# Kernel optimization log

Measured on AMD Instinct MI355X. Metric: run time of the kernel, lower is better.

Reference implementation:

```python
import jax, jax.numpy as jnp
import numpy as np

N_E = 1024
E_DIM = 64
BETA = 0.25
DECAY = 0.99
EPSILON = 1e-5


def setup_inputs() -> dict:
    key = jax.random.key(0)
    k1, k2, k3 = jax.random.split(key, 3)
    z = jax.random.normal(k1, (32, E_DIM, 32, 32), dtype=jnp.float32)
    # codebook initialized uniform(-1/n_e, 1/n_e) as in the torch module
    emb_w = jax.random.uniform(k2, (N_E, E_DIM), minval=-1.0 / N_E, maxval=1.0 / N_E, dtype=jnp.float32)
    ema_cluster_size = jnp.ones((N_E,), dtype=jnp.float32)
    ema_w = jax.random.uniform(k3, (N_E, E_DIM), minval=-1.0 / N_E, maxval=1.0 / N_E, dtype=jnp.float32)
    return {"z": z, "emb_w": emb_w, "ema_cluster_size": ema_cluster_size, "ema_w": ema_w}


def reference(z, emb_w, ema_cluster_size, ema_w):
    B, C, H, W = z.shape  # C == E_DIM
    zf = jnp.transpose(z, (0, 2, 3, 1)).reshape(-1, E_DIM)  # [N, e_dim]
    N = zf.shape[0]

    # squared-distance via ||z||^2 + ||e||^2 - 2 z.e (same expansion as torch code)
    d = (jnp.sum(zf * zf, axis=1, keepdims=True)
         + jnp.sum(emb_w * emb_w, axis=1)
         - 2.0 * zf @ emb_w.T)  # [N, n_e]
    idx = jnp.argmin(d, axis=1)  # [N]

    min_encodings = jax.nn.one_hot(idx, N_E, dtype=jnp.float32)  # [N, n_e]
    # cluster stats via scatter-add (equivalent to one-hot matmuls, cheaper)
    cluster_size = jax.ops.segment_sum(jnp.ones((N,), jnp.float32), idx, num_segments=N_E)
    sum_encodings = jax.ops.segment_sum(zf, idx, num_segments=N_E)  # [n_e, e_dim]

    # EMA update (training path, done before the z_q lookup as in torch)
    new_cs = DECAY * ema_cluster_size + (1.0 - DECAY) * cluster_size
    new_w = DECAY * ema_w + (1.0 - DECAY) * sum_encodings
    n = jnp.sum(new_cs)
    cs_norm = (new_cs + EPSILON) / (n + N_E * EPSILON) * n
    new_emb = new_w / cs_norm[:, None]  # updated codebook

    z_q = new_emb[idx].reshape(B, H, W, C).transpose(0, 3, 1, 2)  # [B,C,H,W]
    loss = BETA * jnp.mean((jax.lax.stop_gradient(z_q) - z) ** 2)
    z_q_st = z + jax.lax.stop_gradient(z_q - z)  # straight-through

    avg_probs = cluster_size / N
    perplexity = jnp.exp(-jnp.sum(avg_probs * jnp.log(avg_probs + 1e-10)))
    return loss, z_q_st, perplexity, min_encodings, idx
```

## Files before the change

### kernel.cpp

```cpp
#include <hip/hip_runtime.h>
#include <math.h>

#define NVEC 32768
#define NE   1024
#define ED   64
#define TOT  2097152
#define NCHUNK 4
#define CHUNK  256
#define MT     128

#define O_LOSS   0
#define O_ZQ     1
#define O_PERP   2097153
#define O_MINENC 2097154
#define O_IDX    35651586

#define W_PIDX   0
#define W_CS     32768
#define W_SUMENC 33792
#define W_NEWEMB 99328
#define W_ESQ    164864


__global__ void __launch_bounds__(256) k_pre(const float* __restrict__ emb,
                                             float* __restrict__ ws,
                                             float* __restrict__ out) {
    int b = blockIdx.x;
    if (b < 65) {
        int i = b * 256 + threadIdx.x;
        float4 zv; zv.x = 0.f; zv.y = 0.f; zv.z = 0.f; zv.w = 0.f;
        *(float4*)(ws + W_CS + i * 4) = zv;
        if (b == 0 && threadIdx.x == 0) out[O_LOSS] = 0.f;
    } else {
        int code = (b - 65) * 256 + threadIdx.x;
        const float* ep = emb + (size_t)code * ED;
        float r[8];
#pragma unroll
        for (int j = 0; j < 8; ++j) r[j] = __fmul_rn(ep[j], ep[j]);
#pragma unroll
        for (int i = 8; i < 64; i += 8)
#pragma unroll
            for (int j = 0; j < 8; ++j)
                r[j] = __fadd_rn(r[j], __fmul_rn(ep[i + j], ep[i + j]));
        ws[W_ESQ + code] = __fadd_rn(
            __fadd_rn(__fadd_rn(r[0], r[1]), __fadd_rn(r[2], r[3])),
            __fadd_rn(__fadd_rn(r[4], r[5]), __fadd_rn(r[6], r[7])));
    }
}

__device__ __forceinline__ int apos(int m) {
    return ((m & 4) << 4) + ((m >> 3) << 2) + (m & 3);
}

__global__ void __launch_bounds__(512) k_dist(const float* __restrict__ z,
                                              const float* __restrict__ emb,
                                              const float* __restrict__ esq_g,
                                              int* __restrict__ fidx,
                                              int* __restrict__ cnt,
                                              float* __restrict__ sumenc,
                                              float* __restrict__ out) {
    __shared__ __align__(16) float s_a[64 * 128];
    __shared__ __align__(16) float s_b[2 * 64 * 132];
    __shared__ float s_esq[CHUNK];
    __shared__ float s_zsq[MT];
    __shared__ int s_bi[MT];

    int tid = threadIdx.x;
    int n0 = blockIdx.x * MT;
    int b = n0 >> 10, hw0 = n0 & 1023;
    const float* zb = z + b * 65536 + hw0;

#pragma unroll
    for (int j = 0; j < 4; ++j) {
        int f4i = j * 512 + tid;
        int q = f4i & 31, c = f4i >> 5;
        float4 v = *(const float4*)(zb + (c << 10) + q * 4);
        v.x = __fmul_rn(2.0f, v.x);
        v.y = __fmul_rn(2.0f, v.y);
        v.z = __fmul_rn(2.0f, v.z);
        v.w = __fmul_rn(2.0f, v.w);
        *(float4*)(s_a + c * 128 + ((q & 1) << 6) + ((q >> 1) << 2)) = v;
    }
    __syncthreads();

    if (tid < MT) {
        int p = apos(tid);
        float r[8];
#pragma unroll
        for (int j = 0; j < 8; ++j) {
            float v = s_a[j * 128 + p];
            r[j] = __fmul_rn(v, v);
        }
#pragma unroll
        for (int i = 8; i < 64; i += 8)
#pragma unroll
            for (int j = 0; j < 8; ++j) {
                float v = s_a[(i + j) * 128 + p];
                r[j] = __fadd_rn(r[j], __fmul_rn(v, v));
            }
        s_zsq[tid] = __fmul_rn(0.25f, __fadd_rn(
            __fadd_rn(__fadd_rn(r[0], r[1]), __fadd_rn(r[2], r[3])),
            __fadd_rn(__fadd_rn(r[4], r[5]), __fadd_rn(r[6], r[7]))));
    }
    __syncthreads();

    int mi = tid & 15, ki = tid >> 4;
    int kbase = ki * 8;
    int kk = ki & 15;
    const float* sbk = s_b + (ki >> 4) * 8448;
    float zs[8];
#pragma unroll
    for (int mu = 0; mu < 8; ++mu) zs[mu] = s_zsq[8 * mi + mu];

    float bd[8];
    int bix[8];
#pragma unroll
    for (int mu = 0; mu < 8; ++mu) { bd[mu] = 3.4e38f; bix[mu] = kbase; }

    for (int ch = 0; ch < NCHUNK; ++ch) {
        int k0 = ch * CHUNK;
        __syncthreads();
#pragma unroll
        for (int j = 0; j < 8; ++j) {
            int f4i = j * 512 + tid;
            int kl = f4i >> 4, c4 = f4i & 15;
            float4 v = *(const float4*)(emb + (size_t)(k0 + kl) * ED + c4 * 4);
            int sc = kl >> 7, klr = kl & 127;
            float* sb = s_b + sc * 8448;
            int base = (((klr >> 2) + c4) & 31) * 4 + (klr & 3);
            sb[(c4 * 4 + 0) * 132 + base] = v.x;
            sb[(c4 * 4 + 1) * 132 + base] = v.y;
            sb[(c4 * 4 + 2) * 132 + base] = v.z;
            sb[(c4 * 4 + 3) * 132 + base] = v.w;
        }
        if (tid < CHUNK) s_esq[tid] = esq_g[k0 + tid];
        __syncthreads();

        float acc[8][8];
#pragma unroll
        for (int mu = 0; mu < 8; ++mu)
#pragma unroll
            for (int ku = 0; ku < 8; ++ku) acc[mu][ku] = 0.f;

#pragma unroll 2
        for (int c = 0; c < 64; ++c) {
            int c4 = c >> 2;
            const float* ar = s_a + c * 128 + (mi << 2);
            float4 a0 = *(const float4*)(ar);
            float4 a1 = *(const float4*)(ar + 64);
            float4 b0 = *(const float4*)(sbk + c * 132 + ((2 * kk + c4) & 31) * 4);
            float4 b1 = *(const float4*)(sbk + c * 132 + ((2 * kk + 1 + c4) & 31) * 4);
#pragma unroll
            for (int mu = 0; mu < 8; ++mu) {
                float a = (mu < 4) ? (&a0.x)[mu] : (&a1.x)[mu - 4];
                acc[mu][0] = __fmaf_rn(a, b0.x, acc[mu][0]);
                acc[mu][1] = __fmaf_rn(a, b0.y, acc[mu][1]);
                acc[mu][2] = __fmaf_rn(a, b0.z, acc[mu][2]);
                acc[mu][3] = __fmaf_rn(a, b0.w, acc[mu][3]);
                acc[mu][4] = __fmaf_rn(a, b1.x, acc[mu][4]);
                acc[mu][5] = __fmaf_rn(a, b1.y, acc[mu][5]);
                acc[mu][6] = __fmaf_rn(a, b1.z, acc[mu][6]);
                acc[mu][7] = __fmaf_rn(a, b1.w, acc[mu][7]);
            }
        }

#pragma unroll
        for (int mu = 0; mu < 8; ++mu)
#pragma unroll
            for (int ku = 0; ku < 8; ++ku) {
                float d = __fsub_rn(__fadd_rn(zs[mu], s_esq[kbase + ku]),
                                    acc[mu][ku]);
                if (d < bd[mu]) { bd[mu] = d; bix[mu] = k0 + kbase + ku; }
            }
    }

    __syncthreads();
    float* red_d = s_b;
    int* red_i = (int*)(s_b + 4096);
#pragma unroll
    for (int mu = 0; mu < 8; ++mu) {
        red_d[ki * 128 + 8 * mi + mu] = bd[mu];
        red_i[ki * 128 + 8 * mi + mu] = bix[mu];
    }
    __syncthreads();
    if (tid < MT) {
        float best = red_d[tid];
        int bi = red_i[tid];
#pragma unroll
        for (int q = 1; q < 32; ++q) {
            float d = red_d[q * 128 + tid];
            int i = red_i[q * 128 + tid];
            if (d < best || (d == best && i < bi)) { best = d; bi = i; }
        }
        fidx[n0 + tid] = bi;
        out[O_IDX + n0 + tid] = (float)bi;
        s_bi[tid] = bi;
        atomicAdd(&cnt[bi], 1);
    }
    __syncthreads();

    {
        int m = tid & 127, qt = tid >> 7;
        int p = apos(m);
#pragma unroll
        for (int j = 0; j < 16; ++j) {
            int c = qt * 16 + j;
            s_b[m * 65 + c] = __fmul_rn(0.5f, s_a[c * 128 + p]);
        }
    }
    __syncthreads();

    {
        int lane = tid & 63, w = tid >> 6;
#pragma unroll
        for (int t = 0; t < 16; ++t) {
            int m = (w << 4) | t;
            int bi = s_bi[m];
            float v = s_b[m * 65 + lane];
            unsafeAtomicAdd(sumenc + ((size_t)bi << 6) + lane, v);
        }
    }
}

__global__ void __launch_bounds__(1024) k_ema(const float* __restrict__ ema_cs,
                                              const float* __restrict__ ema_w,
                                              const int* __restrict__ cnt,
                                              const float* __restrict__ sumenc,
                                              float* __restrict__ newemb,
                                              float* __restrict__ out) {
    int k = threadIdx.x;
    float c = (float)cnt[k];
    float ncs = 0.99f * ema_cs[k] + (1.0f - 0.99f) * c;
    float p = c * (1.0f / (float)NVEC);
    float e = p * logf(p + 1e-10f);
    float rn_ = ncs, re_ = e;
#pragma unroll
    for (int o = 32; o > 0; o >>= 1) {
        rn_ += __shfl_down(rn_, o, 64);
        re_ += __shfl_down(re_, o, 64);
    }
    __shared__ float sn[16], se_[16];
    __shared__ float s_n;
    int wave = k >> 6, lane = k & 63;
    if (lane == 0) { sn[wave] = rn_; se_[wave] = re_; }
    __syncthreads();
    if (k == 0) {
        float tn = 0.f, te = 0.f;
#pragma unroll
        for (int w = 0; w < 16; ++w) { tn += sn[w]; te += se_[w]; }
        s_n = tn;
        out[O_PERP] = expf(-te);
    }
    __syncthreads();
    float nt = s_n;
    float csn = (ncs + 1e-5f) / (nt + 1024.0f * 1e-5f) * nt;
    __shared__ float s_csn[NE];
    s_csn[k] = csn;
    __syncthreads();
    const float4* w4 = (const float4*)ema_w;
    const float4* s4 = (const float4*)sumenc;
    float4* n4 = (float4*)newemb;
#pragma unroll 4
    for (int it = 0; it < 16; ++it) {
        int t4 = it * 1024 + k;
        float4 w = w4[t4];
        float4 s = s4[t4];
        float cs_ = s_csn[t4 >> 4];
        float4 o;
        o.x = (0.99f * w.x + (1.0f - 0.99f) * s.x) / cs_;
        o.y = (0.99f * w.y + (1.0f - 0.99f) * s.y) / cs_;
        o.z = (0.99f * w.z + (1.0f - 0.99f) * s.z) / cs_;
        o.w = (0.99f * w.w + (1.0f - 0.99f) * s.w) / cs_;
        n4[t4] = o;
    }
}

__global__ void __launch_bounds__(256) k_zq(const float* __restrict__ z,
                                            const int* __restrict__ idx,
                                            const float* __restrict__ newemb,
                                            float* __restrict__ out) {
    __shared__ int sbi[16];
    if (threadIdx.x < 16) sbi[threadIdx.x] = idx[blockIdx.x * 16 + threadIdx.x];
    __syncthreads();

    float local = 0.f;
#pragma unroll
    for (int i = 0; i < 4; ++i) {
        int t = blockIdx.x * 256 + threadIdx.x + i * 524288;
        int b = t >> 16, c = (t >> 10) & 63, hw = t & 1023;
        int n = (b << 10) | hw;
        float e = newemb[idx[n] * ED + c];
        float zv = z[t];
        float diff = e - zv;
        out[O_ZQ + t] = zv + diff;
        local = fmaf(diff, diff, local);
    }

    int t = threadIdx.x;
    int r0 = blockIdx.x * 16;
    for (int r = 0; r < 16; ++r) {
        int rbi = sbi[r];
        float* rp = out + O_MINENC + (size_t)(r0 + r) * NE;
        if (t < 254) {
            int col = 2 + t * 4;
            float4 v;
            v.x = (col == rbi) ? 1.0f : 0.0f;
            v.y = (col + 1 == rbi) ? 1.0f : 0.0f;
            v.z = (col + 2 == rbi) ? 1.0f : 0.0f;
            v.w = (col + 3 == rbi) ? 1.0f : 0.0f;
            *(float4*)(rp + col) = v;
        } else if (t == 254) {
            float2 v;
            v.x = (0 == rbi) ? 1.0f : 0.0f;
            v.y = (1 == rbi) ? 1.0f : 0.0f;
            *(float2*)(rp) = v;
        } else {
            float4 v;
            v.x = (1018 == rbi) ? 1.0f : 0.0f;
            v.y = (1019 == rbi) ? 1.0f : 0.0f;
            v.z = (1020 == rbi) ? 1.0f : 0.0f;
            v.w = (1021 == rbi) ? 1.0f : 0.0f;
            *(float4*)(rp + 1018) = v;
            float2 w;
            w.x = (1022 == rbi) ? 1.0f : 0.0f;
            w.y = (1023 == rbi) ? 1.0f : 0.0f;
            *(float2*)(rp + 1022) = w;
        }
    }

#pragma unroll
    for (int o = 32; o > 0; o >>= 1) local += __shfl_down(local, o, 64);
    __shared__ float sp[4];
    int wave = threadIdx.x >> 6;
    if ((threadIdx.x & 63) == 0) sp[wave] = local;
    __syncthreads();
    if (threadIdx.x == 0)
        unsafeAtomicAdd(out + O_LOSS,
                        ((sp[0] + sp[1]) + (sp[2] + sp[3])) * (0.25f / (float)TOT));
}

extern "C" void kernel_launch(void* const* d_in, const int* in_sizes, int n_in,
                              void* d_out, int out_size, void* d_ws, size_t ws_size,
                              hipStream_t stream) {
    const float* z      = (const float*)d_in[0];
    const float* emb    = (const float*)d_in[1];
    const float* ema_cs = (const float*)d_in[2];
    const float* ema_w  = (const float*)d_in[3];
    float* out = (float*)d_out;
    float* ws  = (float*)d_ws;

    k_pre<<<69, 256, 0, stream>>>(emb, ws, out);
    k_dist<<<NVEC / MT, 512, 0, stream>>>(z, emb, ws + W_ESQ, (int*)(ws + W_PIDX),
                                          (int*)(ws + W_CS), ws + W_SUMENC, out);
    k_ema<<<1, 1024, 0, stream>>>(ema_cs, ema_w, (const int*)(ws + W_CS),
                                  ws + W_SUMENC, ws + W_NEWEMB, out);
    k_zq<<<2048, 256, 0, stream>>>(z, (const int*)(ws + W_PIDX), ws + W_NEWEMB,
                                   out);
}
```

Before: 258.6 us.

## Fuse EMA codebook update into z_q kernel and batch LDS loads in distance GEMM

Removes the single-block k_ema launch by having every k_zq block recompute the cluster-size normalisation (1024 counts, a reduction and logs) and form the updated codebook entries on the fly from ema_w and sumenc. This drops one serial kernel, its launch gap, and the newemb workspace round trip. In exchange, each of 2048 blocks redoes the 1024-entry reduction and reads two arrays per gathered element instead of one. Separately, the distance inner loop now loads four channels of A/B fragments from shared memory before the FMAs, to give more load-latency hiding at some register cost.

```diff
diff --git a/kernel.cpp b/kernel.cpp
--- a/kernel.cpp
+++ b/kernel.cpp
@@ -18,7 +18,6 @@
 #define W_PIDX   0
 #define W_CS     32768
 #define W_SUMENC 33792
-#define W_NEWEMB 99328
 #define W_ESQ    164864
 
 
@@ -142,25 +141,32 @@
 #pragma unroll
             for (int ku = 0; ku < 8; ++ku) acc[mu][ku] = 0.f;
 
-#pragma unroll 2
-        for (int c = 0; c < 64; ++c) {
-            int c4 = c >> 2;
-            const float* ar = s_a + c * 128 + (mi << 2);
-            float4 a0 = *(const float4*)(ar);
-            float4 a1 = *(const float4*)(ar + 64);
-            float4 b0 = *(const float4*)(sbk + c * 132 + ((2 * kk + c4) & 31) * 4);
-            float4 b1 = *(const float4*)(sbk + c * 132 + ((2 * kk + 1 + c4) & 31) * 4);
-#pragma unroll
-            for (int mu = 0; mu < 8; ++mu) {
-                float a = (mu < 4) ? (&a0.x)[mu] : (&a1.x)[mu - 4];
-                acc[mu][0] = __fmaf_rn(a, b0.x, acc[mu][0]);
-                acc[mu][1] = __fmaf_rn(a, b0.y, acc[mu][1]);
-                acc[mu][2] = __fmaf_rn(a, b0.z, acc[mu][2]);
-                acc[mu][3] = __fmaf_rn(a, b0.w, acc[mu][3]);
-                acc[mu][4] = __fmaf_rn(a, b1.x, acc[mu][4]);
-                acc[mu][5] = __fmaf_rn(a, b1.y, acc[mu][5]);
-                acc[mu][6] = __fmaf_rn(a, b1.z, acc[mu][6]);
-                acc[mu][7] = __fmaf_rn(a, b1.w, acc[mu][7]);
+        for (int cg = 0; cg < 64; cg += 4) {
+            float4 A0[4], A1[4], B0[4], B1[4];
+#pragma unroll
+            for (int j = 0; j < 4; ++j) {
+                int c = cg + j;
+                int c4 = c >> 2;
+                const float* ar = s_a + c * 128 + (mi << 2);
+                A0[j] = *(const float4*)(ar);
+                A1[j] = *(const float4*)(ar + 64);
+                B0[j] = *(const float4*)(sbk + c * 132 + ((2 * kk + c4) & 31) * 4);
+                B1[j] = *(const float4*)(sbk + c * 132 + ((2 * kk + 1 + c4) & 31) * 4);
+            }
+#pragma unroll
+            for (int j = 0; j < 4; ++j) {
+#pragma unroll
+                for (int mu = 0; mu < 8; ++mu) {
+                    float a = (mu < 4) ? (&A0[j].x)[mu] : (&A1[j].x)[mu - 4];
+                    acc[mu][0] = __fmaf_rn(a, B0[j].x, acc[mu][0]);
+                    acc[mu][1] = __fmaf_rn(a, B0[j].y, acc[mu][1]);
+                    acc[mu][2] = __fmaf_rn(a, B0[j].z, acc[mu][2]);
+                    acc[mu][3] = __fmaf_rn(a, B0[j].w, acc[mu][3]);
+                    acc[mu][4] = __fmaf_rn(a, B1[j].x, acc[mu][4]);
+                    acc[mu][5] = __fmaf_rn(a, B1[j].y, acc[mu][5]);
+                    acc[mu][6] = __fmaf_rn(a, B1[j].z, acc[mu][6]);
+                    acc[mu][7] = __fmaf_rn(a, B1[j].w, acc[mu][7]);
+                }
             }
         }
 
@@ -222,81 +228,67 @@
     }
 }
 
-__global__ void __launch_bounds__(1024) k_ema(const float* __restrict__ ema_cs,
-                                              const float* __restrict__ ema_w,
-                                              const int* __restrict__ cnt,
-                                              const float* __restrict__ sumenc,
-                                              float* __restrict__ newemb,
-                                              float* __restrict__ out) {
-    int k = threadIdx.x;
-    float c = (float)cnt[k];
-    float ncs = 0.99f * ema_cs[k] + (1.0f - 0.99f) * c;
-    float p = c * (1.0f / (float)NVEC);
-    float e = p * logf(p + 1e-10f);
-    float rn_ = ncs, re_ = e;
-#pragma unroll
-    for (int o = 32; o > 0; o >>= 1) {
-        rn_ += __shfl_down(rn_, o, 64);
-        re_ += __shfl_down(re_, o, 64);
-    }
-    __shared__ float sn[16], se_[16];
-    __shared__ float s_n;
-    int wave = k >> 6, lane = k & 63;
-    if (lane == 0) { sn[wave] = rn_; se_[wave] = re_; }
-    __syncthreads();
-    if (k == 0) {
-        float tn = 0.f, te = 0.f;
-#pragma unroll
-        for (int w = 0; w < 16; ++w) { tn += sn[w]; te += se_[w]; }
-        s_n = tn;
-        out[O_PERP] = expf(-te);
-    }
-    __syncthreads();
-    float nt = s_n;
-    float csn = (ncs + 1e-5f) / (nt + 1024.0f * 1e-5f) * nt;
-    __shared__ float s_csn[NE];
-    s_csn[k] = csn;
-    __syncthreads();
-    const float4* w4 = (const float4*)ema_w;
-    const float4* s4 = (const float4*)sumenc;
-    float4* n4 = (float4*)newemb;
-#pragma unroll 4
-    for (int it = 0; it < 16; ++it) {
-        int t4 = it * 1024 + k;
-        float4 w = w4[t4];
-        float4 s = s4[t4];
-        float cs_ = s_csn[t4 >> 4];
-        float4 o;
-        o.x = (0.99f * w.x + (1.0f - 0.99f) * s.x) / cs_;
-        o.y = (0.99f * w.y + (1.0f - 0.99f) * s.y) / cs_;
-        o.z = (0.99f * w.z + (1.0f - 0.99f) * s.z) / cs_;
-        o.w = (0.99f * w.w + (1.0f - 0.99f) * s.w) / cs_;
-        n4[t4] = o;
-    }
-}
-
 __global__ void __launch_bounds__(256) k_zq(const float* __restrict__ z,
                                             const int* __restrict__ idx,
-                                            const float* __restrict__ newemb,
+                                            const float* __restrict__ ema_cs,
+                                            const float* __restrict__ ema_w,
+                                            const int* __restrict__ cnt,
+                                            const float* __restrict__ sumenc,
                                             float* __restrict__ out) {
+    __shared__ float s_csn[NE];
+    __shared__ float swn[4], swe[4];
     __shared__ int sbi[16];
-    if (threadIdx.x < 16) sbi[threadIdx.x] = idx[blockIdx.x * 16 + threadIdx.x];
+    int tid = threadIdx.x;
+
+    float myncs[4];
+    float rn = 0.f, re = 0.f;
+#pragma unroll
+    for (int j = 0; j < 4; ++j) {
+        int k = j * 256 + tid;
+        float c = (float)cnt[k];
+        float ncs = 0.99f * ema_cs[k] + (1.0f - 0.99f) * c;
+        myncs[j] = ncs;
+        rn += ncs;
+        float p = c * (1.0f / (float)NVEC);
+        re += p * logf(p + 1e-10f);
+    }
+#pragma unroll
+    for (int o = 32; o > 0; o >>= 1) {
+        rn += __shfl_down(rn, o, 64);
+        re += __shfl_down(re, o, 64);
+    }
+    int wave = tid >> 6;
+    if ((tid & 63) == 0) { swn[wave] = rn; swe[wave] = re; }
+    if (tid < 16) sbi[tid] = idx[blockIdx.x * 16 + tid];
+    __syncthreads();
+    float nt = (swn[0] + swn[1]) + (swn[2] + swn[3]);
+    if (blockIdx.x == 0 && tid == 0) {
+        float te = (swe[0] + swe[1]) + (swe[2] + swe[3]);
+        out[O_PERP] = expf(-te);
+    }
+#pragma unroll
+    for (int j = 0; j < 4; ++j) {
+        int k = j * 256 + tid;
+        s_csn[k] = (myncs[j] + 1e-5f) / (nt + 1024.0f * 1e-5f) * nt;
+    }
     __syncthreads();
 
     float local = 0.f;
 #pragma unroll
     for (int i = 0; i < 4; ++i) {
-        int t = blockIdx.x * 256 + threadIdx.x + i * 524288;
+        int t = blockIdx.x * 256 + tid + i * 524288;
         int b = t >> 16, c = (t >> 10) & 63, hw = t & 1023;
         int n = (b << 10) | hw;
-        float e = newemb[idx[n] * ED + c];
+        int g = idx[n] * ED + c;
+        float nw = 0.99f * ema_w[g] + (1.0f - 0.99f) * sumenc[g];
+        float e = nw / s_csn[g >> 6];
         float zv = z[t];
         float diff = e - zv;
         out[O_ZQ + t] = zv + diff;
         local = fmaf(diff, diff, local);
     }
 
-    int t = threadIdx.x;
+    int t = tid;
     int r0 = blockIdx.x * 16;
     for (int r = 0; r < 16; ++r) {
         int rbi = sbi[r];
@@ -331,10 +323,9 @@
 #pragma unroll
     for (int o = 32; o > 0; o >>= 1) local += __shfl_down(local, o, 64);
     __shared__ float sp[4];
-    int wave = threadIdx.x >> 6;
-    if ((threadIdx.x & 63) == 0) sp[wave] = local;
-    __syncthreads();
-    if (threadIdx.x == 0)
+    if ((tid & 63) == 0) sp[wave] = local;
+    __syncthreads();
+    if (tid == 0)
         unsafeAtomicAdd(out + O_LOSS,
                         ((sp[0] + sp[1]) + (sp[2] + sp[3])) * (0.25f / (float)TOT));
 }
@@ -352,8 +343,6 @@
     k_pre<<<69, 256, 0, stream>>>(emb, ws, out);
     k_dist<<<NVEC / MT, 512, 0, stream>>>(z, emb, ws + W_ESQ, (int*)(ws + W_PIDX),
                                           (int*)(ws + W_CS), ws + W_SUMENC, out);
-    k_ema<<<1, 1024, 0, stream>>>(ema_cs, ema_w, (const int*)(ws + W_CS),
-                                  ws + W_SUMENC, ws + W_NEWEMB, out);
-    k_zq<<<2048, 256, 0, stream>>>(z, (const int*)(ws + W_PIDX), ws + W_NEWEMB,
-                                   out);
-}
+    k_zq<<<2048, 256, 0, stream>>>(z, (const int*)(ws + W_PIDX), ema_cs, ema_w,
+                                   (const int*)(ws + W_CS), ws + W_SUMENC, out);
+}
```

Measured after the change: 243.1 us. 1.06x faster.
